# Kernel optimization log

Measured on AMD Instinct MI355X. Metric: run time of the kernel, lower is better.

## Reference

```python
import jax, jax.numpy as jnp
import numpy as np

N = 50000          # neuron_count
NNZ = 1_600_000    # edges (avg degree 32)
B = 32             # batch
L = 3              # CONNECTOME_LAYER_NUMBER


def setup_inputs() -> dict:
    key = jax.random.key(0)
    k1, k2, k3, k4, k5 = jax.random.split(key, 5)
    x = jax.random.normal(k1, (B, N), dtype=jnp.float32)
    adj_vals = jax.random.uniform(k2, (NNZ,), dtype=jnp.float32)
    w_vals = jax.random.uniform(k3, (NNZ,), dtype=jnp.float32)
    bias = jnp.ones((N,), dtype=jnp.float32)
    row = jax.random.randint(k4, (NNZ,), 0, N, dtype=jnp.int32)
    col = jax.random.randint(k5, (NNZ,), 0, N, dtype=jnp.int32)
    return {"x": x, "adj_vals": adj_vals, "w_vals": w_vals, "bias": bias,
            "row": row, "col": col}


def _spmm(vals, row, col, dense, n):
    # (sparse NxN) @ dense [N, B] via gather + segment_sum scatter
    contrib = vals[:, None] * dense[col]          # [nnz, B]
    return jax.ops.segment_sum(contrib, row, num_segments=n)


def reference(x, adj_vals, w_vals, bias, row, col):
    # Original per layer: x = ((A @ W) @ x^T)^T + bias.
    # We use associativity: (A @ W) @ x^T == A @ (W @ x^T), avoiding the
    # explicit SpGEMM while computing the same linear map.
    n = bias.shape[0]
    xt = x.T                                      # [N, B]
    for _ in range(L):
        wx = _spmm(w_vals, row, col, xt, n)       # W @ x^T -> [N, B]
        xt = _spmm(adj_vals, row, col, wx, n)     # A @ (W @ x^T)
        xt = xt + bias[:, None]                   # broadcast bias over batch
    return xt.T                                   # [B, N]
```

## Files before the change

kernel.cpp:

```cpp
#include <hip/hip_runtime.h>


#define NN 50000
#define NNZ_E 1600000
#define NB (NN * 32)
#define CHUNK 6144
#define NBLK1 ((NNZ_E + CHUNK - 1) / CHUNK)
#define NBIN ((NN + 127) / 128)
#define NH (NBIN * NBLK1)
#define CAP2 5120
#define BCAP 6144
#define LENP (NBIN * BCAP)
#define SCAN_NBLK ((NH + 255) / 256)

__device__ __forceinline__ int clampi(int v, int hi) {
    v = v < 0 ? 0 : v;
    return v > hi ? hi : v;
}

__device__ __forceinline__ unsigned short f2h(float v) {
    union { _Float16 h; unsigned short u; } cv;
    cv.h = (_Float16)v;
    return cv.u;
}

__device__ __forceinline__ float kv_val(unsigned kv) {
    union { unsigned short u; _Float16 h; } cv;
    cv.u = (unsigned short)(kv >> 16);
    return (float)cv.h;
}

__global__ __launch_bounds__(256) void hist_kernel(const int* __restrict__ row,
                                                   int* __restrict__ hist1) {
    __shared__ int h[NBIN];
    int blk = blockIdx.x, tid = threadIdx.x;
    for (int j = tid; j < NBIN; j += 256) h[j] = 0;
    __syncthreads();
    int base = blk * CHUNK;
    int n = NNZ_E - base; if (n > CHUNK) n = CHUNK;
    for (int i = tid; i < n; i += 256)
        atomicAdd(&h[clampi(row[base + i], NN - 1) >> 7], 1);
    __syncthreads();
    for (int j = tid; j < NBIN; j += 256) hist1[j * NBLK1 + blk] = h[j];
}

__global__ void scan_local_kernel(int* __restrict__ data, int n, int* __restrict__ bsum) {
    __shared__ int s[256];
    int i = blockIdx.x * 256 + threadIdx.x;
    int v = (i < n) ? data[i] : 0;
    s[threadIdx.x] = v;
    __syncthreads();
    for (int off = 1; off < 256; off <<= 1) {
        int t = (threadIdx.x >= off) ? s[threadIdx.x - off] : 0;
        __syncthreads();
        s[threadIdx.x] += t;
        __syncthreads();
    }
    if (i < n) data[i] = s[threadIdx.x] - v;
    if (threadIdx.x == 255) bsum[blockIdx.x] = s[threadIdx.x];
}

__global__ void scan_tops_kernel(int* __restrict__ bsum, int m) {
    __shared__ int s[512];
    int t = threadIdx.x;
    int v = (t < m) ? bsum[t] : 0;
    s[t] = v;
    __syncthreads();
    for (int off = 1; off < 512; off <<= 1) {
        int u = (t >= off) ? s[t - off] : 0;
        __syncthreads();
        s[t] += u;
        __syncthreads();
    }
    if (t < m) bsum[t] = s[t] - v;
}

__global__ void fin_add_kernel(int* __restrict__ data, int n, const int* __restrict__ bsum) {
    int i = blockIdx.x * blockDim.x + threadIdx.x;
    if (i < n) data[i] += bsum[i >> 8];
}

__global__ void binstart_kernel(const int* __restrict__ hist1, int* __restrict__ binstart) {
    int j = blockIdx.x * blockDim.x + threadIdx.x;
    if (j < NBIN) binstart[j] = hist1[j * NBLK1];
    if (j == 0) binstart[NBIN] = NNZ_E;
}

__global__ __launch_bounds__(256) void pass1_kernel(
        const int* __restrict__ row, const int* __restrict__ col,
        const float* __restrict__ a, const float* __restrict__ w,
        const int* __restrict__ hist1_off,
        unsigned* __restrict__ k1, unsigned* __restrict__ aw1) {
    __shared__ int h[NBIN];
    __shared__ int hscan[NBIN];
    __shared__ int hoff[NBIN];
    __shared__ int s256[256];
    __shared__ unsigned sKey[CHUNK];
    __shared__ unsigned sAW[CHUNK];
    int blk = blockIdx.x, tid = threadIdx.x;
    int base = blk * CHUNK;
    int n = NNZ_E - base; if (n > CHUNK) n = CHUNK;

    for (int j = tid; j < NBIN; j += 256) {
        h[j] = 0;
        hoff[j] = hist1_off[j * NBLK1 + blk];
    }
    __syncthreads();
    for (int i = tid; i < n; i += 256)
        atomicAdd(&h[clampi(row[base + i], NN - 1) >> 7], 1);
    __syncthreads();
    int j0 = tid * 2, j1 = tid * 2 + 1;
    int c0 = (j0 < NBIN) ? h[j0] : 0;
    int c1 = (j1 < NBIN) ? h[j1] : 0;
    int tsum = c0 + c1;
    s256[tid] = tsum;
    __syncthreads();
    for (int off = 1; off < 256; off <<= 1) {
        int t = (tid >= off) ? s256[tid - off] : 0;
        __syncthreads();
        s256[tid] += t;
        __syncthreads();
    }
    int ex = s256[tid] - tsum;
    __syncthreads();
    if (j0 < NBIN) { hscan[j0] = ex;      h[j0] = ex; }
    if (j1 < NBIN) { hscan[j1] = ex + c0; h[j1] = ex + c0; }
    __syncthreads();
    for (int i = tid; i < n; i += 256) {
        int r = clampi(row[base + i], NN - 1);
        int c = clampi(col[base + i], NN - 1);
        int bin = r >> 7;
        int p = atomicAdd(&h[bin], 1);
        p = clampi(p, n - 1);
        sKey[p] = ((unsigned)r << 16) | (unsigned)c;
        sAW[p] = ((unsigned)f2h(a[base + i]) << 16) | (unsigned)f2h(w[base + i]);
    }
    __syncthreads();
    for (int p = tid; p < n; p += 256) {
        unsigned key = sKey[p];
        int bin = (int)(key >> 23);
        int d = clampi(hoff[bin] + (p - hscan[bin]), NNZ_E - 1);
        k1[d] = key;
        aw1[d] = sAW[p];
    }
}

__global__ __launch_bounds__(256) void pass2_kernel(
        const unsigned* __restrict__ k1, const unsigned* __restrict__ aw1,
        const int* __restrict__ binstart,
        unsigned* __restrict__ kvA2, unsigned* __restrict__ kvW2,
        unsigned* __restrict__ row_desc) {
    __shared__ unsigned sKey[CAP2];
    __shared__ unsigned sAW[CAP2];
    __shared__ int rh[128];
    __shared__ int rs[128];
    __shared__ int cur[128];
    int bin = blockIdx.x, tid = threadIdx.x;
    int r0 = bin << 7;
    int rows = NN - r0; if (rows > 128) rows = 128;
    int base = clampi(binstart[bin], NNZ_E);
    int size = clampi(binstart[bin + 1], NNZ_E) - base;
    size = clampi(size, CAP2);
    int pbase = bin * BCAP;

    if (tid < 128) rh[tid] = 0;
    __syncthreads();
    for (int i = tid; i < size; i += 256) {
        unsigned key = k1[base + i];
        atomicAdd(&rh[(key >> 16) & 127], 1);
        sKey[i] = key;
        sAW[i] = aw1[base + i];
    }
    __syncthreads();
    int cnt  = (tid < 128) ? rh[tid] : 0;
    int plen = (cnt + 7) & ~7;
    if (tid < 128) rs[tid] = plen;
    __syncthreads();
    for (int off = 1; off < 128; off <<= 1) {
        int t = (tid >= off && tid < 128) ? rs[tid - off] : 0;
        __syncthreads();
        if (tid < 128) rs[tid] += t;
        __syncthreads();
    }
    int rofs = (tid < 128) ? clampi(rs[tid] - plen, BCAP - 8) : 0;
    if (tid < 128) cur[tid] = rofs;
    if (tid < rows)
        row_desc[r0 + tid] = (unsigned)(pbase + rofs) | ((unsigned)(plen >> 3) << 24);
    __syncthreads();
    for (int i = tid; i < size; i += 256) {
        unsigned key = sKey[i];
        unsigned aw  = sAW[i];
        int rl = (key >> 16) & 127;
        int p = atomicAdd(&cur[rl], 1);
        p = clampi(p, BCAP - 1);
        unsigned c = key & 0xFFFFu;
        kvA2[pbase + p] = (aw & 0xFFFF0000u) | c;
        kvW2[pbase + p] = (aw << 16) | c;
    }
    __syncthreads();
    if (tid < rows) {
        int pl = (rh[tid] + 7) & ~7;
        for (int q = rh[tid]; q < pl; ++q) {
            int d = clampi(rofs + q, BCAP - 1);
            kvA2[pbase + d] = 0u;
            kvW2[pbase + d] = 0u;
        }
    }
}

__global__ void transpose_in_kernel(const float* __restrict__ x,
                                    _Float16* __restrict__ xt) {
    int i = blockIdx.x * blockDim.x + threadIdx.x;
    if (i < NB) {
        int n = i >> 5;
        int b = i & 31;
        xt[i] = (_Float16)x[b * NN + n];
    }
}

template <int WITH_BIAS>
__global__ __launch_bounds__(256) void spmm_kernel(
        const uint2* __restrict__ kv2, const unsigned* __restrict__ row_desc,
        const unsigned* __restrict__ in32, unsigned* __restrict__ out32,
        const float* __restrict__ bias, float outScale, float biasScale) {
    int t = blockIdx.x * 256 + threadIdx.x;
    int r = t >> 4;
    int l = t & 15;
    if (r >= NN) return;
    unsigned d = row_desc[r];
    int niter = (int)(d >> 24);
    int base2 = clampi((int)(d & 0xFFFFFFu), LENP - 8) >> 1;
    float accL = 0.0f, accH = 0.0f;
    uint2 k2[4];
    if (niter > 0) {
#pragma unroll
        for (int q = 0; q < 4; ++q) k2[q] = kv2[base2 + q];
    }
    for (int it = 0; it < niter; ++it) {
        unsigned k[8];
#pragma unroll
        for (int q = 0; q < 4; ++q) { k[2 * q] = k2[q].x; k[2 * q + 1] = k2[q].y; }
        unsigned gd[8];
#pragma unroll
        for (int j = 0; j < 8; ++j) gd[j] = in32[((k[j] & 0xFFFFu) << 4) + l];
        if (it + 1 < niter) {
            int nb2 = base2 + (it + 1) * 4;
#pragma unroll
            for (int q = 0; q < 4; ++q) k2[q] = kv2[nb2 + q];
        }
#pragma unroll
        for (int j = 0; j < 8; ++j) {
            float v = kv_val(k[j]);
            union { unsigned u; _Float16 h[2]; } cv;
            cv.u = gd[j];
            accL += v * (float)cv.h[0];
            accH += v * (float)cv.h[1];
        }
    }
    float rL = accL * outScale, rH = accH * outScale;
    if (WITH_BIAS) {
        float bb = bias[r] * biasScale;
        rL += bb; rH += bb;
    }
    union { unsigned u; _Float16 h[2]; } o;
    o.h[0] = (_Float16)rL;
    o.h[1] = (_Float16)rH;
    out32[(r << 4) + l] = o.u;
}

__global__ void transpose_out_kernel(const _Float16* __restrict__ xt,
                                     float* __restrict__ out) {
    int i = blockIdx.x * blockDim.x + threadIdx.x;
    if (i < NB) {
        int b = i / NN;
        int n = i - b * NN;
        out[i] = (float)xt[(n << 5) + b] * 16777216.0f;
    }
}

extern "C" void kernel_launch(void* const* d_in, const int* in_sizes, int n_in,
                              void* d_out, int out_size, void* d_ws, size_t ws_size,
                              hipStream_t stream) {
    const float* x        = (const float*)d_in[0];
    const float* adj_vals = (const float*)d_in[1];
    const float* w_vals   = (const float*)d_in[2];
    const float* bias     = (const float*)d_in[3];
    const int*   row      = (const int*)d_in[4];
    const int*   col      = (const int*)d_in[5];
    float* out = (float*)d_out;

    unsigned*  k1        = (unsigned*)d_ws;
    unsigned*  aw1       = k1 + NNZ_E;
    unsigned*  kvA2      = aw1 + NNZ_E;
    unsigned*  kvW2      = kvA2 + LENP;
    _Float16*  xt16      = (_Float16*)(kvW2 + LENP);
    _Float16*  tmp16     = xt16 + NB;
    int*   hist1         = (int*)(tmp16 + NB);
    int*   bsumB         = hist1 + NH;
    int*   binstart      = bsumB + 512;
    unsigned* row_desc   = (unsigned*)(binstart + NBIN + 8);

    const int BS = 256;
    const int grid_nb   = (NB + BS - 1) / BS;
    const int grid_spmm = (NN * 16 + BS - 1) / BS;

    hist_kernel<<<NBLK1, BS, 0, stream>>>(row, hist1);
    scan_local_kernel<<<SCAN_NBLK, BS, 0, stream>>>(hist1, NH, bsumB);
    scan_tops_kernel<<<1, 512, 0, stream>>>(bsumB, SCAN_NBLK);
    fin_add_kernel<<<SCAN_NBLK, BS, 0, stream>>>(hist1, NH, bsumB);
    binstart_kernel<<<(NBIN + 1 + BS - 1) / BS, BS, 0, stream>>>(hist1, binstart);

    pass1_kernel<<<NBLK1, BS, 0, stream>>>(row, col, adj_vals, w_vals,
                                           hist1, k1, aw1);
    pass2_kernel<<<NBIN, BS, 0, stream>>>(k1, aw1, binstart, kvA2, kvW2, row_desc);

    const uint2* kvA = (const uint2*)kvA2;
    const uint2* kvW = (const uint2*)kvW2;
    const unsigned* xt32  = (const unsigned*)xt16;
    unsigned*       xt32w = (unsigned*)xt16;
    const unsigned* tm32  = (const unsigned*)tmp16;
    unsigned*       tm32w = (unsigned*)tmp16;

    transpose_in_kernel<<<grid_nb, BS, 0, stream>>>(x, xt16);
    const float r256 = 1.0f / 256.0f;
    float biasScale = 1.0f;
    for (int layer = 0; layer < 3; ++layer) {
        biasScale *= r256;
        spmm_kernel<0><<<grid_spmm, BS, 0, stream>>>(kvW, row_desc, xt32, tm32w,
                                                     nullptr, 1.0f, 0.0f);
        spmm_kernel<1><<<grid_spmm, BS, 0, stream>>>(kvA, row_desc, tm32, xt32w,
                                                     bias, r256, biasScale);
    }
    transpose_out_kernel<<<grid_nb, BS, 0, stream>>>(xt16, out);
}
```

Measured before the change: 247.0 us.

## Software-pipeline SpMM gathers one iteration ahead with uint4 index loads

Restructures the SpMM inner loop so the eight dense gathers for the next iteration are issued before the current iteration's FMAs, and key/value words are prefetched two iterations ahead. Index loads are widened from uint2 to uint4, and launch bounds now request 8 blocks per SM. The aim is to hide gather latency behind the accumulation. In exchange it uses more registers, which may conflict with the occupancy hint, and it assumes row bases are 4-aligned for uint4 access.

```diff
diff --git a/kernel.cpp b/kernel.cpp
--- a/kernel.cpp
+++ b/kernel.cpp
@@ -28,6 +28,15 @@
     union { unsigned short u; _Float16 h; } cv;
     cv.u = (unsigned short)(kv >> 16);
     return (float)cv.h;
+}
+
+__device__ __forceinline__ unsigned u4_at(const uint4& v, int j) {
+    switch (j & 3) {
+        case 0: return v.x;
+        case 1: return v.y;
+        case 2: return v.z;
+        default: return v.w;
+    }
 }
 
 __global__ __launch_bounds__(256) void hist_kernel(const int* __restrict__ row,
@@ -219,8 +228,8 @@
 }
 
 template <int WITH_BIAS>
-__global__ __launch_bounds__(256) void spmm_kernel(
-        const uint2* __restrict__ kv2, const unsigned* __restrict__ row_desc,
+__global__ __launch_bounds__(256, 8) void spmm_kernel(
+        const uint4* __restrict__ kv4, const unsigned* __restrict__ row_desc,
         const unsigned* __restrict__ in32, unsigned* __restrict__ out32,
         const float* __restrict__ bias, float outScale, float biasScale) {
     int t = blockIdx.x * 256 + threadIdx.x;
@@ -229,33 +238,41 @@
     if (r >= NN) return;
     unsigned d = row_desc[r];
     int niter = (int)(d >> 24);
-    int base2 = clampi((int)(d & 0xFFFFFFu), LENP - 8) >> 1;
+    int base4 = clampi((int)(d & 0xFFFFFFu), LENP - 8) >> 2;
+    const uint4* kp = kv4 + base4;
     float accL = 0.0f, accH = 0.0f;
-    uint2 k2[4];
+    uint4 kA0, kA1, kB0, kB1;
+    unsigned gC[8], gN[8];
     if (niter > 0) {
+        kA0 = kp[0]; kA1 = kp[1];
 #pragma unroll
-        for (int q = 0; q < 4; ++q) k2[q] = kv2[base2 + q];
+        for (int j = 0; j < 8; ++j) {
+            unsigned kw = u4_at(j < 4 ? kA0 : kA1, j);
+            gC[j] = in32[((kw & 0xFFFFu) << 4) + l];
+        }
+        kB0 = kA0; kB1 = kA1;
+        if (niter > 1) { kB0 = kp[2]; kB1 = kp[3]; }
     }
     for (int it = 0; it < niter; ++it) {
-        unsigned k[8];
+        if (it + 1 < niter) {
 #pragma unroll
-        for (int q = 0; q < 4; ++q) { k[2 * q] = k2[q].x; k[2 * q + 1] = k2[q].y; }
-        unsigned gd[8];
-#pragma unroll
-        for (int j = 0; j < 8; ++j) gd[j] = in32[((k[j] & 0xFFFFu) << 4) + l];
-        if (it + 1 < niter) {
-            int nb2 = base2 + (it + 1) * 4;
-#pragma unroll
-            for (int q = 0; q < 4; ++q) k2[q] = kv2[nb2 + q];
+            for (int j = 0; j < 8; ++j) {
+                unsigned kw = u4_at(j < 4 ? kB0 : kB1, j);
+                gN[j] = in32[((kw & 0xFFFFu) << 4) + l];
+            }
         }
 #pragma unroll
         for (int j = 0; j < 8; ++j) {
-            float v = kv_val(k[j]);
+            float v = kv_val(u4_at(j < 4 ? kA0 : kA1, j));
             union { unsigned u; _Float16 h[2]; } cv;
-            cv.u = gd[j];
+            cv.u = gC[j];
             accL += v * (float)cv.h[0];
             accH += v * (float)cv.h[1];
         }
+        kA0 = kB0; kA1 = kB1;
+        if (it + 2 < niter) { kB0 = kp[(it + 2) * 2]; kB1 = kp[(it + 2) * 2 + 1]; }
+#pragma unroll
+        for (int j = 0; j < 8; ++j) gC[j] = gN[j];
     }
     float rL = accL * outScale, rH = accH * outScale;
     if (WITH_BIAS) {
@@ -314,8 +331,8 @@
                                            hist1, k1, aw1);
     pass2_kernel<<<NBIN, BS, 0, stream>>>(k1, aw1, binstart, kvA2, kvW2, row_desc);
 
-    const uint2* kvA = (const uint2*)kvA2;
-    const uint2* kvW = (const uint2*)kvW2;
+    const uint4* kvA = (const uint4*)kvA2;
+    const uint4* kvW = (const uint4*)kvW2;
     const unsigned* xt32  = (const unsigned*)xt16;
     unsigned*       xt32w = (unsigned*)xt16;
     const unsigned* tm32  = (const unsigned*)tmp16;
```

After: 262.1 us. 1.06x slower.

## Fuse transposes and scan stages into neighboring kernels to cut launches

Applied to the files above, without the earlier changes.

The input transpose now runs in extra blocks of the histogram kernel, and the output transpose is folded into the last SpMM, which writes fp32 output directly in [B,N] layout. The scan-tops, final-add and binstart kernels are merged into one kernel in which every block redundantly rescans the 512 block sums. Together these remove five kernel launches and two standalone passes over the dense arrays. In exchange, the final SpMM does strided scattered stores, and each scan block repeats the small top-level scan.

```diff
diff --git a/kernel.cpp b/kernel.cpp
--- a/kernel.cpp
+++ b/kernel.cpp
@@ -12,6 +12,7 @@
 #define BCAP 6144
 #define LENP (NBIN * BCAP)
 #define SCAN_NBLK ((NH + 255) / 256)
+#define TIN_BLKS 98
 
 __device__ __forceinline__ int clampi(int v, int hi) {
     v = v < 0 ? 0 : v;
@@ -31,9 +32,19 @@
 }
 
 __global__ __launch_bounds__(256) void hist_kernel(const int* __restrict__ row,
-                                                   int* __restrict__ hist1) {
+                                                   int* __restrict__ hist1,
+                                                   const float* __restrict__ x,
+                                                   _Float16* __restrict__ xt) {
     __shared__ int h[NBIN];
     int blk = blockIdx.x, tid = threadIdx.x;
+    if (blk >= NBLK1) {
+        for (int i = (blk - NBLK1) * 256 + tid; i < NB; i += TIN_BLKS * 256) {
+            int n = i >> 5;
+            int b = i & 31;
+            xt[i] = (_Float16)x[b * NN + n];
+        }
+        return;
+    }
     for (int j = tid; j < NBIN; j += 256) h[j] = 0;
     __syncthreads();
     int base = blk * CHUNK;
@@ -60,30 +71,36 @@
     if (threadIdx.x == 255) bsum[blockIdx.x] = s[threadIdx.x];
 }
 
-__global__ void scan_tops_kernel(int* __restrict__ bsum, int m) {
-    __shared__ int s[512];
-    int t = threadIdx.x;
-    int v = (t < m) ? bsum[t] : 0;
-    s[t] = v;
-    __syncthreads();
+__global__ __launch_bounds__(256) void scanfin_kernel(int* __restrict__ data, int n,
+                                                      const int* __restrict__ bsum, int m,
+                                                      int* __restrict__ binstart) {
+    __shared__ int sa[512];
+    __shared__ int sb[512];
+    int tid = threadIdx.x;
+    sa[tid]       = (tid < m) ? bsum[tid] : 0;
+    sa[tid + 256] = (tid + 256 < m) ? bsum[tid + 256] : 0;
+    __syncthreads();
+    int* src = sa;
+    int* dst = sb;
     for (int off = 1; off < 512; off <<= 1) {
-        int u = (t >= off) ? s[t - off] : 0;
-        __syncthreads();
-        s[t] += u;
-        __syncthreads();
-    }
-    if (t < m) bsum[t] = s[t] - v;
-}
-
-__global__ void fin_add_kernel(int* __restrict__ data, int n, const int* __restrict__ bsum) {
-    int i = blockIdx.x * blockDim.x + threadIdx.x;
-    if (i < n) data[i] += bsum[i >> 8];
-}
-
-__global__ void binstart_kernel(const int* __restrict__ hist1, int* __restrict__ binstart) {
-    int j = blockIdx.x * blockDim.x + threadIdx.x;
-    if (j < NBIN) binstart[j] = hist1[j * NBLK1];
-    if (j == 0) binstart[NBIN] = NNZ_E;
+#pragma unroll
+        for (int q = 0; q < 2; ++q) {
+            int p = tid + q * 256;
+            int v = src[p];
+            if (p >= off) v += src[p - off];
+            dst[p] = v;
+        }
+        __syncthreads();
+        int* t = src; src = dst; dst = t;
+    }
+    int add = (blockIdx.x > 0) ? src[blockIdx.x - 1] : 0;
+    int i = blockIdx.x * 256 + tid;
+    if (i < n) {
+        int v = data[i] + add;
+        data[i] = v;
+        if (i % NBLK1 == 0) binstart[i / NBLK1] = v;
+    }
+    if (i == 0) binstart[NBIN] = NNZ_E;
 }
 
 __global__ __launch_bounds__(256) void pass1_kernel(
@@ -208,21 +225,12 @@
     }
 }
 
-__global__ void transpose_in_kernel(const float* __restrict__ x,
-                                    _Float16* __restrict__ xt) {
-    int i = blockIdx.x * blockDim.x + threadIdx.x;
-    if (i < NB) {
-        int n = i >> 5;
-        int b = i & 31;
-        xt[i] = (_Float16)x[b * NN + n];
-    }
-}
-
-template <int WITH_BIAS>
+template <int WITH_BIAS, int FINAL>
 __global__ __launch_bounds__(256) void spmm_kernel(
         const uint2* __restrict__ kv2, const unsigned* __restrict__ row_desc,
         const unsigned* __restrict__ in32, unsigned* __restrict__ out32,
-        const float* __restrict__ bias, float outScale, float biasScale) {
+        const float* __restrict__ bias, float outScale, float biasScale,
+        float* __restrict__ outf) {
     int t = blockIdx.x * 256 + threadIdx.x;
     int r = t >> 4;
     int l = t & 15;
@@ -262,19 +270,14 @@
         float bb = bias[r] * biasScale;
         rL += bb; rH += bb;
     }
-    union { unsigned u; _Float16 h[2]; } o;
-    o.h[0] = (_Float16)rL;
-    o.h[1] = (_Float16)rH;
-    out32[(r << 4) + l] = o.u;
-}
-
-__global__ void transpose_out_kernel(const _Float16* __restrict__ xt,
-                                     float* __restrict__ out) {
-    int i = blockIdx.x * blockDim.x + threadIdx.x;
-    if (i < NB) {
-        int b = i / NN;
-        int n = i - b * NN;
-        out[i] = (float)xt[(n << 5) + b] * 16777216.0f;
+    if (FINAL) {
+        outf[(2 * l) * NN + r]     = rL * 16777216.0f;
+        outf[(2 * l + 1) * NN + r] = rH * 16777216.0f;
+    } else {
+        union { unsigned u; _Float16 h[2]; } o;
+        o.h[0] = (_Float16)rL;
+        o.h[1] = (_Float16)rH;
+        out32[(r << 4) + l] = o.u;
     }
 }
 
@@ -301,14 +304,11 @@
     unsigned* row_desc   = (unsigned*)(binstart + NBIN + 8);
 
     const int BS = 256;
-    const int grid_nb   = (NB + BS - 1) / BS;
     const int grid_spmm = (NN * 16 + BS - 1) / BS;
 
-    hist_kernel<<<NBLK1, BS, 0, stream>>>(row, hist1);
+    hist_kernel<<<NBLK1 + TIN_BLKS, BS, 0, stream>>>(row, hist1, x, xt16);
     scan_local_kernel<<<SCAN_NBLK, BS, 0, stream>>>(hist1, NH, bsumB);
-    scan_tops_kernel<<<1, 512, 0, stream>>>(bsumB, SCAN_NBLK);
-    fin_add_kernel<<<SCAN_NBLK, BS, 0, stream>>>(hist1, NH, bsumB);
-    binstart_kernel<<<(NBIN + 1 + BS - 1) / BS, BS, 0, stream>>>(hist1, binstart);
+    scanfin_kernel<<<SCAN_NBLK, BS, 0, stream>>>(hist1, NH, bsumB, SCAN_NBLK, binstart);
 
     pass1_kernel<<<NBLK1, BS, 0, stream>>>(row, col, adj_vals, w_vals,
                                            hist1, k1, aw1);
@@ -321,15 +321,17 @@
     const unsigned* tm32  = (const unsigned*)tmp16;
     unsigned*       tm32w = (unsigned*)tmp16;
 
-    transpose_in_kernel<<<grid_nb, BS, 0, stream>>>(x, xt16);
     const float r256 = 1.0f / 256.0f;
-    float biasScale = 1.0f;
-    for (int layer = 0; layer < 3; ++layer) {
-        biasScale *= r256;
-        spmm_kernel<0><<<grid_spmm, BS, 0, stream>>>(kvW, row_desc, xt32, tm32w,
-                                                     nullptr, 1.0f, 0.0f);
-        spmm_kernel<1><<<grid_spmm, BS, 0, stream>>>(kvA, row_desc, tm32, xt32w,
-                                                     bias, r256, biasScale);
-    }
-    transpose_out_kernel<<<grid_nb, BS, 0, stream>>>(xt16, out);
-}
+    spmm_kernel<0, 0><<<grid_spmm, BS, 0, stream>>>(kvW, row_desc, xt32, tm32w,
+                                                    nullptr, 1.0f, 0.0f, nullptr);
+    spmm_kernel<1, 0><<<grid_spmm, BS, 0, stream>>>(kvA, row_desc, tm32, xt32w,
+                                                    bias, r256, 1.0f / 256.0f, nullptr);
+    spmm_kernel<0, 0><<<grid_spmm, BS, 0, stream>>>(kvW, row_desc, xt32, tm32w,
+                                                    nullptr, 1.0f, 0.0f, nullptr);
+    spmm_kernel<1, 0><<<grid_spmm, BS, 0, stream>>>(kvA, row_desc, tm32, xt32w,
+                                                    bias, r256, 1.0f / 65536.0f, nullptr);
+    spmm_kernel<0, 0><<<grid_spmm, BS, 0, stream>>>(kvW, row_desc, xt32, tm32w,
+                                                    nullptr, 1.0f, 0.0f, nullptr);
+    spmm_kernel<1, 1><<<grid_spmm, BS, 0, stream>>>(kvA, row_desc, tm32, xt32w,
+                                                    bias, r256, 1.0f / 16777216.0f, out);
+}
```

New measurement: 241.7 us. 1.02x faster.
